# Kernel tuning notes

Hardware: AMD Instinct MI355X
Metric: run time of the kernel (lower is better)

Reference implementation:

```python
import jax, jax.numpy as jnp
import numpy as np

# Config (mirrors init_kwargs)
B, S = 1, 2048          # batch, seq_len
H = 2048                # hidden_size
NH, NKV = 16, 8         # attention heads, kv heads (GQA n_rep = 2)
HD = H // NH            # head_dim = 128
I = 5632                # intermediate_size
L = 2                   # num_hidden_layers
V = 32000               # vocab_size
WIN = 1024              # sliding_window
THETA = 10000.0
EPS = 1e-6


def setup_inputs() -> dict:
    key = jax.random.key(0)
    ks = jax.random.split(key, 12)
    s = 0.02
    return {
        "input_ids": jax.random.randint(ks[0], (B, S), 0, V, dtype=jnp.int32),
        "embed": jax.random.normal(ks[1], (V, H), jnp.float32) * s,
        "Wq": jax.random.normal(ks[2], (L, H, NH * HD), jnp.float32) * s,
        "Wk": jax.random.normal(ks[3], (L, H, NKV * HD), jnp.float32) * s,
        "Wv": jax.random.normal(ks[4], (L, H, NKV * HD), jnp.float32) * s,
        "Wo": jax.random.normal(ks[5], (L, NH * HD, H), jnp.float32) * s,
        "Wg": jax.random.normal(ks[6], (L, H, I), jnp.float32) * s,
        "Wu": jax.random.normal(ks[7], (L, H, I), jnp.float32) * s,
        "Wd": jax.random.normal(ks[8], (L, I, H), jnp.float32) * s,
        "ln1": jnp.ones((L, H), jnp.float32),
        "ln2": jnp.ones((L, H), jnp.float32),
        "norm_w": jnp.ones((H,), jnp.float32),
    }


def _rmsnorm(x, w, eps=EPS):
    return x * jax.lax.rsqrt(jnp.mean(x * x, axis=-1, keepdims=True) + eps) * w


def _rope_tables(seq_len, dim, theta):
    inv_freq = 1.0 / (theta ** (jnp.arange(0, dim, 2, dtype=jnp.float32) / dim))
    freqs = jnp.arange(seq_len, dtype=jnp.float32)[:, None] * inv_freq[None, :]  # [S, dim/2]
    emb = jnp.concatenate([freqs, freqs], axis=-1)  # [S, dim]
    return jnp.cos(emb), jnp.sin(emb)


def _rotate_half(x):
    half = x.shape[-1] // 2
    return jnp.concatenate([-x[..., half:], x[..., :half]], axis=-1)


def _sliding_window_causal_mask(seq_len, window, dtype):
    i = jnp.arange(seq_len)[:, None]
    j = jnp.arange(seq_len)[None, :]
    allowed = (j <= i) & (j >= i - window)  # band: causal + sliding window
    return jnp.where(allowed, 0.0, jnp.finfo(dtype).min).astype(dtype)[None, None]  # [1,1,S,S]


def _forward(input_ids, embed, Wq, Wk, Wv, Wo, Wg, Wu, Wd, ln1, ln2, norm_w):
    x = embed[input_ids]  # [B,S,H]
    cos, sin = _rope_tables(S, HD, THETA)          # [S,HD]
    cos = cos[None, :, None, :]                    # [1,S,1,HD]
    sin = sin[None, :, None, :]
    mask = _sliding_window_causal_mask(S, WIN, x.dtype)  # [1,1,S,S]
    scale = 1.0 / jnp.sqrt(jnp.float32(HD)).astype(x.dtype)
    n_rep = NH // NKV

    for l in range(L):
        # --- attention block ---
        h = _rmsnorm(x, ln1[l])
        q = (h @ Wq[l]).reshape(B, S, NH, HD)
        k = (h @ Wk[l]).reshape(B, S, NKV, HD)
        v = (h @ Wv[l]).reshape(B, S, NKV, HD)
        q = q * cos + _rotate_half(q) * sin
        k = k * cos + _rotate_half(k) * sin
        # repeat_kv (GQA)
        k = jnp.broadcast_to(k[:, :, :, None, :], (B, S, NKV, n_rep, HD)).reshape(B, S, NH, HD)
        v = jnp.broadcast_to(v[:, :, :, None, :], (B, S, NKV, n_rep, HD)).reshape(B, S, NH, HD)
        scores = jnp.einsum('bshn,bthn->bhst', q, k) * scale + mask  # [B,NH,S,S]
        attn = jax.nn.softmax(scores.astype(jnp.float32), axis=-1).astype(x.dtype)
        o = jnp.einsum('bhst,bthn->bshn', attn, v).reshape(B, S, NH * HD)
        x = x + o @ Wo[l]
        # --- MLP block (SwiGLU) ---
        h = _rmsnorm(x, ln2[l])
        x = x + (jax.nn.silu(h @ Wg[l]) * (h @ Wu[l])) @ Wd[l]

    return _rmsnorm(x, norm_w)


def reference(input_ids, embed, Wq, Wk, Wv, Wo, Wg, Wu, Wd, ln1, ln2, norm_w):
    return _forward(input_ids, embed, Wq, Wk, Wv, Wo, Wg, Wu, Wd, ln1, ln2, norm_w)
```

## Files before the change

### kernel.cpp

```cpp
#include <hip/hip_runtime.h>
#include <stdint.h>

using bf16x8 = __attribute__((ext_vector_type(8))) __bf16;
using f32x4  = __attribute__((ext_vector_type(4))) float;

#define DEVI __device__ __forceinline__

DEVI unsigned short f2b(float f) {
  unsigned int u = __builtin_bit_cast(unsigned int, f);
  u = (u + 0x7FFFu + ((u >> 16) & 1u)) >> 16;
  return (unsigned short)u;
}
DEVI float b2f(unsigned short h) {
  unsigned int u = ((unsigned int)h) << 16;
  return __builtin_bit_cast(float, u);
}
DEVI f32x4 mfma16(bf16x8 a, bf16x8 b, f32x4 c) {
  return __builtin_amdgcn_mfma_f32_16x16x32_bf16(a, b, c, 0, 0, 0);
}
#define GLD(gp, lp) __builtin_amdgcn_global_load_lds( \
    (__attribute__((address_space(1))) void*)(uintptr_t)(gp), \
    (__attribute__((address_space(3))) void*)(uintptr_t)(lp), 16, 0, 0)

static constexpr int S_LEN = 2048;
static constexpr int HDIM  = 2048;
static constexpr int NH    = 16;
static constexpr int NKV   = 8;
static constexpr int HD    = 128;
static constexpr int IFF   = 5632;
static constexpr int WIN   = 1024;

DEVI void rms_finish(float4 v0, float4 v1, const float* __restrict__ w,
                     void* __restrict__ outp, int s, int t, int outf32) {
  float ss = v0.x*v0.x + v0.y*v0.y + v0.z*v0.z + v0.w*v0.w +
             v1.x*v1.x + v1.y*v1.y + v1.z*v1.z + v1.w*v1.w;
  #pragma unroll
  for (int off = 32; off >= 1; off >>= 1) ss += __shfl_xor(ss, off, 64);
  __shared__ float red[4];
  if ((t & 63) == 0) red[t >> 6] = ss;
  __syncthreads();
  ss = red[0] + red[1] + red[2] + red[3];
  float rr = rsqrtf(ss * (1.0f / 2048.0f) + 1e-6f);
  const float4* w4 = (const float4*)w;
  float4 w0 = w4[t], w1 = w4[t + 256];
  float o0x = v0.x*rr*w0.x, o0y = v0.y*rr*w0.y, o0z = v0.z*rr*w0.z, o0w = v0.w*rr*w0.w;
  float o1x = v1.x*rr*w1.x, o1y = v1.y*rr*w1.y, o1z = v1.z*rr*w1.z, o1w = v1.w*rr*w1.w;
  if (outf32) {
    float4* o4 = (float4*)outp + (size_t)s * 512;
    o4[t]       = make_float4(o0x, o0y, o0z, o0w);
    o4[t + 256] = make_float4(o1x, o1y, o1z, o1w);
  } else {
    uint2* ob = (uint2*)((unsigned short*)outp + (size_t)s * HDIM);
    ob[t]       = make_uint2((unsigned)f2b(o0x) | ((unsigned)f2b(o0y) << 16),
                             (unsigned)f2b(o0z) | ((unsigned)f2b(o0w) << 16));
    ob[t + 256] = make_uint2((unsigned)f2b(o1x) | ((unsigned)f2b(o1y) << 16),
                             (unsigned)f2b(o1z) | ((unsigned)f2b(o1w) << 16));
  }
}

__global__ __launch_bounds__(256) void gather_kernel(const int* __restrict__ ids,
    const float* __restrict__ embed, float* __restrict__ x,
    float* __restrict__ ct, float* __restrict__ st,
    const float* __restrict__ ln1w, unsigned short* __restrict__ h) {
  int s = blockIdx.x, t = threadIdx.x;
  const float4* src = (const float4*)(embed + (size_t)ids[s] * HDIM);
  float4* dst = (float4*)(x + (size_t)s * HDIM);
  float4 v0 = src[t], v1 = src[t + 256];
  dst[t]       = v0;
  dst[t + 256] = v1;
  if (t < 64) {
    float inv = expf(-(float)t * (9.210340371976184f / 64.0f));
    float f = (float)s * inv;
    ct[s * 64 + t] = cosf(f);
    st[s * 64 + t] = sinf(f);
  }
  rms_finish(v0, v1, ln1w, h, s, t, 0);
}

template<int OUTF32, int NPARTS>
__global__ __launch_bounds__(256) void rmsnorm_combine_kernel(
    float* __restrict__ x, const float* __restrict__ parts,
    const float* __restrict__ w, void* __restrict__ outp) {
  int s = blockIdx.x, t = threadIdx.x;
  const size_t PS = (size_t)2048 * 2048;
  float4* row = (float4*)(x + (size_t)s * HDIM);
  float4 v0 = row[t], v1 = row[t + 256];
  #pragma unroll
  for (int p = 0; p < NPARTS; ++p) {
    const float4* pr = (const float4*)(parts + p * PS + (size_t)s * HDIM);
    float4 a = pr[t], b = pr[t + 256];
    v0.x += a.x; v0.y += a.y; v0.z += a.z; v0.w += a.w;
    v1.x += b.x; v1.y += b.y; v1.z += b.z; v1.w += b.w;
  }
  row[t] = v0; row[t + 256] = v1;
  rms_finish(v0, v1, w, outp, s, t, OUTF32);
}

__global__ __launch_bounds__(256) void posttrans_kernel(const unsigned short* __restrict__ qkvb,
    const float* __restrict__ ct, const float* __restrict__ st,
    unsigned short* __restrict__ qo, unsigned short* __restrict__ ko,
    unsigned short* __restrict__ vt) {
  __shared__ float tl[64 * 65];
  int b = blockIdx.x;
  if (b < 2048) {
    int s = b, t = threadIdx.x;
    #pragma unroll
    for (int it = 0; it < 6; ++it) {
      int idx = it * 256 + t;
      int head = idx >> 6, d = idx & 63;
      float c = ct[s * 64 + d], sn = st[s * 64 + d];
      if (head < NH) {
        const unsigned short* base = qkvb + (size_t)s * 4096 + head * HD;
        float a = b2f(base[d]), bb = b2f(base[d + 64]);
        unsigned short* dst = qo + (size_t)s * (NH * HD) + head * HD;
        dst[d]      = f2b(a * c - bb * sn);
        dst[d + 64] = f2b(bb * c + a * sn);
      } else {
        int kh = head - NH;
        const unsigned short* base = qkvb + (size_t)s * 4096 + 2048 + kh * HD;
        float a = b2f(base[d]), bb = b2f(base[d + 64]);
        unsigned short* dst = ko + (size_t)s * (NKV * HD) + kh * HD;
        dst[d]      = f2b(a * c - bb * sn);
        dst[d + 64] = f2b(bb * c + a * sn);
      }
    }
  } else {
    int t = b - 2048;
    int k0 = (t / 16) * 64, n0 = (t % 16) * 64;
    int tx = threadIdx.x & 63, ty = threadIdx.x >> 6;
    const unsigned short* in = qkvb + 3072;
    #pragma unroll
    for (int i = 0; i < 16; ++i)
      tl[(ty + 4 * i) * 65 + tx] = b2f(in[(size_t)(k0 + ty + 4 * i) * 4096 + (n0 + tx)]);
    __syncthreads();
    #pragma unroll
    for (int i = 0; i < 16; ++i)
      vt[(size_t)(n0 + ty + 4 * i) * 2048 + (k0 + tx)] = f2b(tl[tx * 65 + (ty + 4 * i)]);
  }
}

__global__ __launch_bounds__(256) void convert_weights_kernel(
    const float* __restrict__ Wq, const float* __restrict__ Wk,
    const float* __restrict__ Wv, const float* __restrict__ Wo,
    const float* __restrict__ Wg, const float* __restrict__ Wu,
    const float* __restrict__ Wd,
    unsigned short* wqkvT, unsigned short* woT,
    unsigned short* wguT, unsigned short* wdT) {
  __shared__ float tl[128 * 65];
  int b = blockIdx.x;
  const float* in; unsigned short* out; int istr, ostr, tilesN, t; int guAdd = -1;
  if (b < 512)       { in = Wq; out = wqkvT;                       istr = 2048; ostr = 2048; tilesN = 32; t = b; }
  else if (b < 768)  { in = Wk; out = wqkvT + (size_t)2048 * 2048; istr = 1024; ostr = 2048; tilesN = 16; t = b - 512; }
  else if (b < 1024) { in = Wv; out = wqkvT + (size_t)3072 * 2048; istr = 1024; ostr = 2048; tilesN = 16; t = b - 768; }
  else if (b < 1536) { in = Wo; out = woT;                         istr = 2048; ostr = 2048; tilesN = 32; t = b - 1024; }
  else if (b < 2944) { in = Wg; out = wguT;                        istr = 5632; ostr = 2048; tilesN = 88; t = b - 1536; guAdd = 0; }
  else if (b < 4352) { in = Wu; out = wguT;                        istr = 5632; ostr = 2048; tilesN = 88; t = b - 2944; guAdd = 128; }
  else               { in = Wd; out = wdT;                         istr = 2048; ostr = 5632; tilesN = 32; t = b - 4352; }
  int k0 = (t / tilesN) * 128, n0 = (t % tilesN) * 64;
  int tx = threadIdx.x & 63, ty = threadIdx.x >> 6;
  #pragma unroll
  for (int i = 0; i < 32; ++i)
    tl[(ty + 4 * i) * 65 + tx] = in[(size_t)(k0 + ty + 4 * i) * istr + (n0 + tx)];
  __syncthreads();
  int ob = (guAdd >= 0) ? (((n0 >> 7) << 8) + (n0 & 64) + guAdd) : n0;
  unsigned int* ou = (unsigned int*)out;
  const int kstr2 = ostr >> 1;
  #pragma unroll
  for (int i = 0; i < 16; ++i) {
    int nrow = ty + 4 * i;
    float lo = tl[(2 * tx) * 65 + nrow], hi = tl[(2 * tx + 1) * 65 + nrow];
    ou[(size_t)(ob + nrow) * kstr2 + (k0 >> 1) + tx] =
        (unsigned int)f2b(lo) | ((unsigned int)f2b(hi) << 16);
  }
}

DEVI bf16x8 ldsAB(const unsigned short* buf, int r, int cbyte) {
  return *(const bf16x8*)((const unsigned char*)buf + r * 128 + (cbyte ^ ((r & 7) << 4)));
}
DEVI void stage_unit(const unsigned short* __restrict__ G, int Kstr,
                     unsigned short* lbuf, int loff0, int grow0,
                     int loff1, int grow1, int w, int l) {
  const int rsub = l >> 3;
  const int ce = ((l & 7) ^ rsub) << 3;
  const unsigned short* s0 = G + (size_t)(grow0 + w * 8 + rsub) * Kstr + ce;
  GLD(s0, (unsigned char*)lbuf + loff0 + w * 1024 + l * 16);
  const unsigned short* s1 = G + (size_t)(grow1 + w * 8 + rsub) * Kstr + ce;
  GLD(s1, (unsigned char*)lbuf + loff1 + w * 1024 + l * 16);
}
template<int Q>
DEVI void phase128(const unsigned short* Ab, f32x4 (&acc)[4][4],
                   bf16x8 (&breg)[2][4], int wr, int lg, int li) {
  const int r0 = wr * 64 + Q * 16 + li;
  bf16x8 a0 = ldsAB(Ab, r0, lg * 16);
  bf16x8 a1 = ldsAB(Ab, r0, 64 + lg * 16);
  __builtin_amdgcn_s_setprio(1);
  #pragma unroll
  for (int n = 0; n < 4; ++n) acc[Q][n] = mfma16(a0, breg[0][n], acc[Q][n]);
  #pragma unroll
  for (int n = 0; n < 4; ++n) acc[Q][n] = mfma16(a1, breg[1][n], acc[Q][n]);
  __builtin_amdgcn_s_setprio(0);
}

template<int EPI>
__global__ __launch_bounds__(512, 1) void gemm128_kernel(
    const unsigned short* __restrict__ A, const unsigned short* __restrict__ Bt,
    void* __restrict__ Cout, int Kstr, int nt, int parts, int nbm, int ldc,
    long long partStride) {
  __shared__ __align__(16) unsigned char smem[98304];
  unsigned short* As0 = (unsigned short*)smem;
  unsigned short* Bs0 = (unsigned short*)(smem + 32768);
  const int tid = threadIdx.x, l = tid & 63, w = tid >> 6;
  const int lg = l >> 4, li = l & 15;
  const int wr = w >> 2, wc = w & 3;
  const int nb = gridDim.x, qx = nb >> 3;
  const int wg = ((int)blockIdx.x & 7) * qx + ((int)blockIdx.x >> 3);
  const int nbT = nb / parts;
  const int tile = wg % nbT, part = wg / nbT;
  const int m0 = (tile % nbm) * 128, n0 = (tile / nbm) * 256;
  const int kOff = part * (nt << 6);
  const unsigned short* At  = A  + (size_t)m0 * Kstr + kOff;
  const unsigned short* Bto = Bt + (size_t)n0 * Kstr + kOff;
  f32x4 acc[4][4] = {};
  bf16x8 breg[2][4];

  stage_unit(Bto, Kstr, Bs0, 0, 0, 8192, 64, w, l);
  stage_unit(Bto, Kstr, Bs0, 16384, 128, 24576, 192, w, l);
  stage_unit(At,  Kstr, As0, 0, 0, 8192, 64, w, l);
  { int k1 = (nt > 1) ? 64 : 0;
    stage_unit(Bto + k1, Kstr, Bs0 + 16384, 0, 0, 8192, 64, w, l);
    stage_unit(Bto + k1, Kstr, Bs0 + 16384, 16384, 128, 24576, 192, w, l); }
  asm volatile("s_waitcnt vmcnt(4)\n\ts_barrier" ::: "memory");

  for (int t = 0; t < nt; ++t) {
    unsigned short* Ab  = As0 + (t & 1) * 8192;
    unsigned short* Bb  = Bs0 + (t & 1) * 16384;
    unsigned short* Abn = As0 + ((t & 1) ^ 1) * 8192;
    const int kt1 = ((t + 1 < nt) ? t + 1 : nt - 1) << 6;
    const int kt2 = ((t + 2 < nt) ? t + 2 : nt - 1) << 6;
    stage_unit(At + kt1, Kstr, Abn, 0, 0, 8192, 64, w, l);
    #pragma unroll
    for (int ks = 0; ks < 2; ++ks)
      #pragma unroll
      for (int n = 0; n < 4; ++n)
        breg[ks][n] = ldsAB(Bb, wc * 64 + n * 16 + li, ks * 64 + lg * 16);
    asm volatile("s_waitcnt lgkmcnt(0)\n\ts_barrier" ::: "memory");
    phase128<0>(Ab, acc, breg, wr, lg, li);
    stage_unit(Bto + kt2, Kstr, Bb, 0, 0, 8192, 64, w, l);
    phase128<1>(Ab, acc, breg, wr, lg, li);
    stage_unit(Bto + kt2, Kstr, Bb, 16384, 128, 24576, 192, w, l);
    phase128<2>(Ab, acc, breg, wr, lg, li);
    phase128<3>(Ab, acc, breg, wr, lg, li);
    asm volatile("s_waitcnt vmcnt(4) lgkmcnt(0)\n\ts_barrier" ::: "memory");
  }
  asm volatile("s_waitcnt vmcnt(0)" ::: "memory");

  if (EPI == 0) {
    float* C = (float*)Cout + (size_t)part * (size_t)partStride;
    #pragma unroll
    for (int m = 0; m < 4; ++m)
      #pragma unroll
      for (int n = 0; n < 4; ++n) {
        int col = n0 + wc * 64 + n * 16 + li;
        #pragma unroll
        for (int r = 0; r < 4; ++r) {
          int row = m0 + wr * 64 + m * 16 + lg * 4 + r;
          C[(size_t)row * ldc + col] = acc[m][n][r];
        }
      }
  } else if (EPI == 1) {
    unsigned short* C = (unsigned short*)Cout;
    #pragma unroll
    for (int m = 0; m < 4; ++m)
      #pragma unroll
      for (int n = 0; n < 4; ++n) {
        int col = n0 + wc * 64 + n * 16 + li;
        #pragma unroll
        for (int r = 0; r < 4; ++r) {
          int row = m0 + wr * 64 + m * 16 + lg * 4 + r;
          C[(size_t)row * ldc + col] = f2b(acc[m][n][r]);
        }
      }
  } else {
    float* ub = (float*)smem;
    asm volatile("s_barrier" ::: "memory");
    if (wc >= 2) {
      #pragma unroll
      for (int m = 0; m < 4; ++m)
        #pragma unroll
        for (int n = 0; n < 4; ++n) {
          int colL = (wc - 2) * 64 + n * 16 + li;
          #pragma unroll
          for (int r = 0; r < 4; ++r) {
            int rowl = wr * 64 + m * 16 + lg * 4 + r;
            ub[rowl * 128 + colL] = acc[m][n][r];
          }
        }
    }
    asm volatile("s_waitcnt lgkmcnt(0)\n\ts_barrier" ::: "memory");
    if (wc < 2) {
      unsigned short* act = (unsigned short*)Cout;
      const int col0 = n0 >> 1;
      #pragma unroll
      for (int m = 0; m < 4; ++m)
        #pragma unroll
        for (int n = 0; n < 4; ++n) {
          int colL = wc * 64 + n * 16 + li;
          #pragma unroll
          for (int r = 0; r < 4; ++r) {
            int rowl = wr * 64 + m * 16 + lg * 4 + r;
            float g = acc[m][n][r];
            float u = ub[rowl * 128 + colL];
            act[(size_t)(m0 + rowl) * ldc + col0 + colL] =
                f2b(g / (1.0f + __expf(-g)) * u);
          }
        }
    }
  }
}

DEVI void stageKV(const unsigned short* __restrict__ kg,
                  const unsigned short* __restrict__ vtg, int kv, int j0,
                  unsigned short* Kbuf, unsigned short* Vbuf, int w, int l) {
  #pragma unroll
  for (int p = 0; p < 2; ++p) {
    int off = p * 8192 + w * 1024 + l * 16;
    int row = off >> 8;
    int colb = (off & 255) ^ ((row & 7) << 4);
    GLD(kg + (size_t)(j0 + row) * (NKV * HD) + kv * HD + (colb >> 1),
        (unsigned char*)Kbuf + off);
  }
  #pragma unroll
  for (int p = 0; p < 2; ++p) {
    int off = p * 8192 + w * 1024 + l * 16;
    int d = off >> 7;
    int colb = (off & 127) ^ ((d & 7) << 4);
    GLD(vtg + (size_t)(kv * HD + d) * S_LEN + j0 + (colb >> 1),
        (unsigned char*)Vbuf + off);
  }
}

__global__ __launch_bounds__(512) void attn_kernel(
    const unsigned short* __restrict__ qg, const unsigned short* __restrict__ kg,
    const unsigned short* __restrict__ vtg, unsigned short* __restrict__ og) {
  __shared__ __align__(16) unsigned short Kl[2][64 * 128];
  __shared__ __align__(16) unsigned short Vtl[2][128 * 64];
  __shared__ __align__(16) unsigned short Plds[8][16 * 72];
  const int tid = threadIdx.x, l = tid & 63, w = tid >> 6;
  const int lg = l >> 4, li = l & 15;
  const int i0 = blockIdx.x * 64, kv = blockIdx.y;
  const int hq = kv * 2 + (w >> 2);
  const int qr0 = i0 + (w & 3) * 16;
  const float scale = 0.08838834764831845f;

  bf16x8 qf[4];
  {
    const unsigned short* qrow = qg + (size_t)(qr0 + li) * (NH * HD) + hq * HD;
    #pragma unroll
    for (int sl = 0; sl < 4; ++sl)
      qf[sl] = *(const bf16x8*)(qrow + sl * 32 + lg * 8);
  }
  f32x4 oacc[8] = {};
  float mrow[4] = {-1e30f, -1e30f, -1e30f, -1e30f};
  float srow[4] = {0.f, 0.f, 0.f, 0.f};

  int jstart = i0 - WIN; if (jstart < 0) jstart = 0;
  stageKV(kg, vtg, kv, jstart, Kl[0], Vtl[0], w, l);

  int it = 0;
  for (int j0 = jstart; j0 <= i0; j0 += 64, ++it) {
    const int cur = it & 1;
    asm volatile("s_waitcnt vmcnt(0) lgkmcnt(0)\n\ts_barrier" ::: "memory");
    if (j0 + 64 <= i0)
      stageKV(kg, vtg, kv, j0 + 64, Kl[cur ^ 1], Vtl[cur ^ 1], w, l);
    const unsigned short* Klds  = Kl[cur];
    const unsigned short* Vtlds = Vtl[cur];

    f32x4 sacc[4] = {};
    #pragma unroll
    for (int nt = 0; nt < 4; ++nt) {
      int kr = nt * 16 + li;
      #pragma unroll
      for (int sl = 0; sl < 4; ++sl) {
        int cb = (sl * 64 + lg * 16) ^ ((kr & 7) << 4);
        bf16x8 kf = *(const bf16x8*)&Klds[(kr * 256 + cb) >> 1];
        sacc[nt] = mfma16(qf[sl], kf, sacc[nt]);
      }
    }

    float pv[4][4];
    #pragma unroll
    for (int r = 0; r < 4; ++r) {
      int qi = qr0 + lg * 4 + r;
      float sval[4];
      float tm = -1e30f;
      #pragma unroll
      for (int nt = 0; nt < 4; ++nt) {
        int j = j0 + nt * 16 + li;
        bool ok = (j <= qi) && (j + WIN >= qi);
        float sv = ok ? sacc[nt][r] * scale : -1e30f;
        sval[nt] = sv;
        tm = fmaxf(tm, sv);
      }
      #pragma unroll
      for (int off2 = 1; off2 < 16; off2 <<= 1)
        tm = fmaxf(tm, __shfl_xor(tm, off2, 64));
      float mnew = fmaxf(mrow[r], tm);
      float resc = __expf(mrow[r] - mnew);
      mrow[r] = mnew;
      float rs = 0.f;
      #pragma unroll
      for (int nt = 0; nt < 4; ++nt) {
        float p = (sval[nt] > -9e29f) ? __expf(sval[nt] - mnew) : 0.f;
        pv[nt][r] = p;
        rs += p;
      }
      #pragma unroll
      for (int off2 = 1; off2 < 16; off2 <<= 1)
        rs += __shfl_xor(rs, off2, 64);
      srow[r] = srow[r] * resc + rs;
      #pragma unroll
      for (int dt = 0; dt < 8; ++dt) oacc[dt][r] *= resc;
    }

    #pragma unroll
    for (int r = 0; r < 4; ++r)
      #pragma unroll
      for (int nt = 0; nt < 4; ++nt)
        Plds[w][(lg * 4 + r) * 72 + nt * 16 + li] = f2b(pv[nt][r]);
    bf16x8 ap[2];
    #pragma unroll
    for (int ks = 0; ks < 2; ++ks)
      ap[ks] = *(const bf16x8*)&Plds[w][li * 72 + ks * 32 + lg * 8];
    #pragma unroll
    for (int dt = 0; dt < 8; ++dt) {
      int d = dt * 16 + li;
      #pragma unroll
      for (int ks = 0; ks < 2; ++ks) {
        int cb = (ks * 64 + lg * 16) ^ ((d & 7) << 4);
        bf16x8 vf = *(const bf16x8*)&Vtlds[(d * 128 + cb) >> 1];
        oacc[dt] = mfma16(ap[ks], vf, oacc[dt]);
      }
    }
  }

  #pragma unroll
  for (int r = 0; r < 4; ++r) {
    float inv = 1.0f / srow[r];
    int qi = qr0 + lg * 4 + r;
    unsigned short* orow = og + (size_t)qi * (NH * HD) + hq * HD;
    #pragma unroll
    for (int dt = 0; dt < 8; ++dt)
      orow[dt * 16 + li] = f2b(oacc[dt][r] * inv);
  }
}

extern "C" void kernel_launch(void* const* d_in, const int* in_sizes, int n_in,
                              void* d_out, int out_size, void* d_ws, size_t ws_size,
                              hipStream_t stream) {
  const int*   ids   = (const int*)d_in[0];
  const float* embed = (const float*)d_in[1];
  const float* Wq    = (const float*)d_in[2];
  const float* Wk    = (const float*)d_in[3];
  const float* Wv    = (const float*)d_in[4];
  const float* Wo    = (const float*)d_in[5];
  const float* Wg    = (const float*)d_in[6];
  const float* Wu    = (const float*)d_in[7];
  const float* Wd    = (const float*)d_in[8];
  const float* ln1   = (const float*)d_in[9];
  const float* ln2   = (const float*)d_in[10];
  const float* normw = (const float*)d_in[11];

  uint8_t* ws = (uint8_t*)d_ws;
  unsigned short* wqkvT = (unsigned short*)(ws + 0);
  unsigned short* woT   = (unsigned short*)(ws + 16777216ull);
  unsigned short* wguT  = (unsigned short*)(ws + 25165824ull);
  unsigned short* wdT   = (unsigned short*)(ws + 71303168ull);
  float*          x     = (float*)(ws + 94371840ull);
  unsigned short* h     = (unsigned short*)(ws + 111149056ull);
  unsigned short* q     = (unsigned short*)(ws + 119537664ull);
  unsigned short* k     = (unsigned short*)(ws + 127926272ull);
  unsigned short* vt    = (unsigned short*)(ws + 132120576ull);
  unsigned short* o     = (unsigned short*)(ws + 136314880ull);
  unsigned short* act   = (unsigned short*)(ws + 119537664ull);
  float*          pbuf  = (float*)(ws + 144703488ull);
  unsigned short* qkvb  = (unsigned short*)(ws + 144703488ull);
  float*          cost  = (float*)(ws + 213909504ull);
  float*          sint  = (float*)(ws + 214433792ull);
  const long long PSo = 4194304LL;

  gather_kernel<<<2048, 256, 0, stream>>>(ids, embed, x, cost, sint, ln1, h);

  for (int l = 0; l < 2; ++l) {
    convert_weights_kernel<<<5760, 256, 0, stream>>>(
        Wq + (size_t)l * 2048 * 2048, Wk + (size_t)l * 2048 * 1024,
        Wv + (size_t)l * 2048 * 1024, Wo + (size_t)l * 2048 * 2048,
        Wg + (size_t)l * 2048 * 5632, Wu + (size_t)l * 2048 * 5632,
        Wd + (size_t)l * 5632 * 2048,
        wqkvT, woT, wguT, wdT);
    if (l == 1)
      rmsnorm_combine_kernel<0, 2><<<2048, 256, 0, stream>>>(x, pbuf, ln1 + 2048, h);
    gemm128_kernel<1><<<256, 512, 0, stream>>>(h, wqkvT, qkvb, 2048, 32, 1, 16, 4096, 0);
    posttrans_kernel<<<2560, 256, 0, stream>>>(qkvb, cost, sint, q, k, vt);
    attn_kernel<<<dim3(32, 8), 512, 0, stream>>>(q, k, vt, o);
    gemm128_kernel<0><<<256, 512, 0, stream>>>(o, woT, pbuf, 2048, 16, 2, 16, 2048, PSo);
    rmsnorm_combine_kernel<0, 2><<<2048, 256, 0, stream>>>(x, pbuf, ln2 + l * 2048, h);
    gemm128_kernel<3><<<704, 512, 0, stream>>>(h, wguT, act, 2048, 32, 1, 16, 5632, 0);
    gemm128_kernel<0><<<256, 512, 0, stream>>>(act, wdT, pbuf, 5632, 44, 2, 16, 2048, PSo);
  }
  rmsnorm_combine_kernel<1, 2><<<2048, 256, 0, stream>>>(x, pbuf, normw, d_out);
  (void)in_sizes; (void)n_in; (void)out_size; (void)ws_size;
}
```

Baseline: 691.6 us.

## Fuse RoPE and V transpose into QKV GEMM epilogue; store split-K partials as bf16

```diff
diff --git a/kernel.cpp b/kernel.cpp
--- a/kernel.cpp
+++ b/kernel.cpp
@@ -79,7 +79,7 @@
 
 template<int OUTF32, int NPARTS>
 __global__ __launch_bounds__(256) void rmsnorm_combine_kernel(
-    float* __restrict__ x, const float* __restrict__ parts,
+    float* __restrict__ x, const unsigned short* __restrict__ parts,
     const float* __restrict__ w, void* __restrict__ outp) {
   int s = blockIdx.x, t = threadIdx.x;
   const size_t PS = (size_t)2048 * 2048;
@@ -87,56 +87,16 @@
   float4 v0 = row[t], v1 = row[t + 256];
   #pragma unroll
   for (int p = 0; p < NPARTS; ++p) {
-    const float4* pr = (const float4*)(parts + p * PS + (size_t)s * HDIM);
-    float4 a = pr[t], b = pr[t + 256];
-    v0.x += a.x; v0.y += a.y; v0.z += a.z; v0.w += a.w;
-    v1.x += b.x; v1.y += b.y; v1.z += b.z; v1.w += b.w;
+    const unsigned short* pr = parts + p * PS + (size_t)s * HDIM;
+    uint2 a = *(const uint2*)(pr + t * 4);
+    uint2 b = *(const uint2*)(pr + (t + 256) * 4);
+    v0.x += b2f((unsigned short)a.x); v0.y += b2f((unsigned short)(a.x >> 16));
+    v0.z += b2f((unsigned short)a.y); v0.w += b2f((unsigned short)(a.y >> 16));
+    v1.x += b2f((unsigned short)b.x); v1.y += b2f((unsigned short)(b.x >> 16));
+    v1.z += b2f((unsigned short)b.y); v1.w += b2f((unsigned short)(b.y >> 16));
   }
   row[t] = v0; row[t + 256] = v1;
   rms_finish(v0, v1, w, outp, s, t, OUTF32);
-}
-
-__global__ __launch_bounds__(256) void posttrans_kernel(const unsigned short* __restrict__ qkvb,
-    const float* __restrict__ ct, const float* __restrict__ st,
-    unsigned short* __restrict__ qo, unsigned short* __restrict__ ko,
-    unsigned short* __restrict__ vt) {
-  __shared__ float tl[64 * 65];
-  int b = blockIdx.x;
-  if (b < 2048) {
-    int s = b, t = threadIdx.x;
-    #pragma unroll
-    for (int it = 0; it < 6; ++it) {
-      int idx = it * 256 + t;
-      int head = idx >> 6, d = idx & 63;
-      float c = ct[s * 64 + d], sn = st[s * 64 + d];
-      if (head < NH) {
-        const unsigned short* base = qkvb + (size_t)s * 4096 + head * HD;
-        float a = b2f(base[d]), bb = b2f(base[d + 64]);
-        unsigned short* dst = qo + (size_t)s * (NH * HD) + head * HD;
-        dst[d]      = f2b(a * c - bb * sn);
-        dst[d + 64] = f2b(bb * c + a * sn);
-      } else {
-        int kh = head - NH;
-        const unsigned short* base = qkvb + (size_t)s * 4096 + 2048 + kh * HD;
-        float a = b2f(base[d]), bb = b2f(base[d + 64]);
-        unsigned short* dst = ko + (size_t)s * (NKV * HD) + kh * HD;
-        dst[d]      = f2b(a * c - bb * sn);
-        dst[d + 64] = f2b(bb * c + a * sn);
-      }
-    }
-  } else {
-    int t = b - 2048;
-    int k0 = (t / 16) * 64, n0 = (t % 16) * 64;
-    int tx = threadIdx.x & 63, ty = threadIdx.x >> 6;
-    const unsigned short* in = qkvb + 3072;
-    #pragma unroll
-    for (int i = 0; i < 16; ++i)
-      tl[(ty + 4 * i) * 65 + tx] = b2f(in[(size_t)(k0 + ty + 4 * i) * 4096 + (n0 + tx)]);
-    __syncthreads();
-    #pragma unroll
-    for (int i = 0; i < 16; ++i)
-      vt[(size_t)(n0 + ty + 4 * i) * 2048 + (k0 + tx)] = f2b(tl[tx * 65 + (ty + 4 * i)]);
-  }
 }
 
 __global__ __launch_bounds__(256) void convert_weights_kernel(
@@ -205,8 +165,10 @@
 __global__ __launch_bounds__(512, 1) void gemm128_kernel(
     const unsigned short* __restrict__ A, const unsigned short* __restrict__ Bt,
     void* __restrict__ Cout, int Kstr, int nt, int parts, int nbm, int ldc,
-    long long partStride) {
-  __shared__ __align__(16) unsigned char smem[98304];
+    long long partStride,
+    const float* __restrict__ ct, const float* __restrict__ st,
+    unsigned short* __restrict__ ko, unsigned short* __restrict__ vt) {
+  __shared__ __align__(16) unsigned char smem[131072];
   unsigned short* As0 = (unsigned short*)smem;
   unsigned short* Bs0 = (unsigned short*)(smem + 32768);
   const int tid = threadIdx.x, l = tid & 63, w = tid >> 6;
@@ -255,20 +217,7 @@
   asm volatile("s_waitcnt vmcnt(0)" ::: "memory");
 
   if (EPI == 0) {
-    float* C = (float*)Cout + (size_t)part * (size_t)partStride;
-    #pragma unroll
-    for (int m = 0; m < 4; ++m)
-      #pragma unroll
-      for (int n = 0; n < 4; ++n) {
-        int col = n0 + wc * 64 + n * 16 + li;
-        #pragma unroll
-        for (int r = 0; r < 4; ++r) {
-          int row = m0 + wr * 64 + m * 16 + lg * 4 + r;
-          C[(size_t)row * ldc + col] = acc[m][n][r];
-        }
-      }
-  } else if (EPI == 1) {
-    unsigned short* C = (unsigned short*)Cout;
+    unsigned short* C = (unsigned short*)Cout + (size_t)part * (size_t)partStride;
     #pragma unroll
     for (int m = 0; m < 4; ++m)
       #pragma unroll
@@ -280,7 +229,7 @@
           C[(size_t)row * ldc + col] = f2b(acc[m][n][r]);
         }
       }
-  } else {
+  } else if (EPI == 3) {
     float* ub = (float*)smem;
     asm volatile("s_barrier" ::: "memory");
     if (wc >= 2) {
@@ -315,6 +264,55 @@
           }
         }
     }
+  } else {
+    float* dump = (float*)smem;
+    asm volatile("s_barrier" ::: "memory");
+    #pragma unroll
+    for (int m = 0; m < 4; ++m)
+      #pragma unroll
+      for (int n = 0; n < 4; ++n) {
+        int colL = wc * 64 + n * 16 + li;
+        #pragma unroll
+        for (int r = 0; r < 4; ++r) {
+          int rowl = wr * 64 + m * 16 + lg * 4 + r;
+          dump[rowl * 256 + colL] = acc[m][n][r];
+        }
+      }
+    asm volatile("s_waitcnt lgkmcnt(0)\n\ts_barrier" ::: "memory");
+    if (n0 < 3072) {
+      unsigned short* qk = (n0 < 2048) ? (unsigned short*)Cout : ko;
+      const int cbase = (n0 < 2048) ? n0 : (n0 - 2048);
+      const int ostr  = (n0 < 2048) ? 2048 : 1024;
+      #pragma unroll
+      for (int m = 0; m < 4; ++m)
+        #pragma unroll
+        for (int n = 0; n < 4; ++n) {
+          int colL = wc * 64 + n * 16 + li;
+          int hi = colL & 64;
+          #pragma unroll
+          for (int r = 0; r < 4; ++r) {
+            int rowl = wr * 64 + m * 16 + lg * 4 + r;
+            int s = m0 + rowl;
+            float own = dump[rowl * 256 + colL];
+            float par = dump[rowl * 256 + (colL ^ 64)];
+            float c  = ct[s * 64 + (colL & 63)];
+            float sn = st[s * 64 + (colL & 63)];
+            float v = hi ? (own * c + par * sn) : (own * c - par * sn);
+            qk[(size_t)s * ostr + cbase + colL] = f2b(v);
+          }
+        }
+    } else {
+      int vcol = tid >> 1, sh = (tid & 1) * 64;
+      unsigned short* dstp = vt + (size_t)(n0 - 3072 + vcol) * 2048 + m0 + sh;
+      #pragma unroll
+      for (int c8 = 0; c8 < 8; ++c8) {
+        unsigned short pk[8];
+        #pragma unroll
+        for (int i = 0; i < 8; ++i)
+          pk[i] = f2b(dump[(sh + c8 * 8 + i) * 256 + vcol]);
+        *(uint4*)(dstp + c8 * 8) = *(const uint4*)pk;
+      }
+    }
   }
 }
 
@@ -482,11 +480,10 @@
   unsigned short* vt    = (unsigned short*)(ws + 132120576ull);
   unsigned short* o     = (unsigned short*)(ws + 136314880ull);
   unsigned short* act   = (unsigned short*)(ws + 119537664ull);
-  float*          pbuf  = (float*)(ws + 144703488ull);
-  unsigned short* qkvb  = (unsigned short*)(ws + 144703488ull);
+  unsigned short* pbuf  = (unsigned short*)(ws + 144703488ull);
   float*          cost  = (float*)(ws + 213909504ull);
   float*          sint  = (float*)(ws + 214433792ull);
-  const long long PSo = 4194304LL;
+  const long long PSel = 4194304LL;
 
   gather_kernel<<<2048, 256, 0, stream>>>(ids, embed, x, cost, sint, ln1, h);
 
@@ -499,13 +496,16 @@
         wqkvT, woT, wguT, wdT);
     if (l == 1)
       rmsnorm_combine_kernel<0, 2><<<2048, 256, 0, stream>>>(x, pbuf, ln1 + 2048, h);
-    gemm128_kernel<1><<<256, 512, 0, stream>>>(h, wqkvT, qkvb, 2048, 32, 1, 16, 4096, 0);
-    posttrans_kernel<<<2560, 256, 0, stream>>>(qkvb, cost, sint, q, k, vt);
+    gemm128_kernel<4><<<256, 512, 0, stream>>>(h, wqkvT, q, 2048, 32, 1, 16, 2048, 0,
+                                               cost, sint, k, vt);
     attn_kernel<<<dim3(32, 8), 512, 0, stream>>>(q, k, vt, o);
-    gemm128_kernel<0><<<256, 512, 0, stream>>>(o, woT, pbuf, 2048, 16, 2, 16, 2048, PSo);
+    gemm128_kernel<0><<<256, 512, 0, stream>>>(o, woT, pbuf, 2048, 16, 2, 16, 2048, PSel,
+                                               nullptr, nullptr, nullptr, nullptr);
     rmsnorm_combine_kernel<0, 2><<<2048, 256, 0, stream>>>(x, pbuf, ln2 + l * 2048, h);
-    gemm128_kernel<3><<<704, 512, 0, stream>>>(h, wguT, act, 2048, 32, 1, 16, 5632, 0);
-    gemm128_kernel<0><<<256, 512, 0, stream>>>(act, wdT, pbuf, 5632, 44, 2, 16, 2048, PSo);
+    gemm128_kernel<3><<<704, 512, 0, stream>>>(h, wguT, act, 2048, 32, 1, 16, 5632, 0,
+                                               nullptr, nullptr, nullptr, nullptr);
+    gemm128_kernel<0><<<256, 512, 0, stream>>>(act, wdT, pbuf, 5632, 44, 2, 16, 2048, PSel,
+                                               nullptr, nullptr, nullptr, nullptr);
   }
   rmsnorm_combine_kernel<1, 2><<<2048, 256, 0, stream>>>(x, pbuf, normw, d_out);
   (void)in_sizes; (void)n_in; (void)out_size; (void)ws_size;
```

Measured after the change: 677.2 us. -2.1%, faster.
